# Performance work log

Hardware: AMD Instinct MI355X
Metric: run time of the kernel (lower is better)

Reference implementation:

```python
import jax, jax.numpy as jnp
import numpy as np

D_MODEL = 256
NHEAD = 8
NLAYERS = 4
DFF = 1024
PATCH = 8
INPUT = 32
C = 2
DATA_DIM = C * PATCH * PATCH  # 128
P = (INPUT // PATCH) ** 2     # 16
NEG = -1.0e6                  # _neg_large_for_dtype(float32)
EPS = 1e-5


def _ln(x, w, b):
    m = x.mean(-1, keepdims=True)
    v = ((x - m) ** 2).mean(-1, keepdims=True)
    return (x - m) / jnp.sqrt(v + EPS) * w + b


def _forward(img_baseline, acq_dts_float, nan_token, pad_embed, emb_w, emb_b, spatial_pos,
             t_w1, t_b1, t_w2, t_b2, t_w3, t_b3,
             in_proj_w, in_proj_b, out_proj_w, out_proj_b,
             lin1_w, lin1_b, lin2_w, lin2_b, norm1_w, norm1_b, norm2_w, norm2_b,
             mean_w1, mean_b1, mean_w2, mean_b2, lv_w1, lv_b1, lv_w2, lv_b2):
    B, T, Cc, Hh, Ww = img_baseline.shape
    p = PATCH
    gh, gw = Hh // p, Ww // p
    L = T * P
    frame_pad = jnp.all(img_baseline == -9999.0, axis=(2, 3, 4))  # (B,T)
    nan_pix = jnp.isnan(img_baseline)
    token = jnp.clip(nan_token, -10.0, 10.0).reshape(1, 1, Cc, 1, 1)
    x = jnp.clip(jnp.where(nan_pix, token, img_baseline), -10.0, 10.0)

    def patchify(a):  # b t c (h ph)(w pw) -> b t (h w) (c ph pw)
        return a.reshape(B, T, Cc, gh, p, gw, p).transpose(0, 1, 3, 5, 2, 4, 6).reshape(B, T, P, Cc * p * p)

    xp = patchify(x)
    seq_nan = patchify(nan_pix).all(-1).reshape(B, L)
    seq_pad = jnp.broadcast_to(frame_pad[:, :, None], (B, T, P)).reshape(B, L)

    # temporal MLP embedding
    t_in = jnp.where(jnp.isnan(acq_dts_float), 0.0, acq_dts_float)[..., None]  # (B,T,1)
    h = jax.nn.relu(t_in @ t_w1.T + t_b1)
    h = jax.nn.relu(h @ t_w2.T + t_b2)
    temb = h @ t_w3.T + t_b3  # (B,T,D)

    z = xp @ emb_w.T + emb_b + spatial_pos + temb[:, :, None, :]  # (B,T,P,D)
    z = z.reshape(B, L, D_MODEL)
    z = jnp.where(seq_pad[..., None], pad_embed, z)  # masked_scatter of pad_embed

    # additive attention mask: rows with NaN/pad patches are fully masked except diagonal
    masked_rows = seq_nan | seq_pad
    mask = jnp.broadcast_to(jnp.where(masked_rows[:, :, None], NEG, 0.0), (B, L, L))
    eye = jnp.eye(L, dtype=bool)
    mask = jnp.where(eye[None, :, :] & masked_rows[:, :, None], 0.0, mask)
    # key_padding_mask merged additively on key columns
    mask = mask + jnp.where(seq_pad[:, None, :], NEG, 0.0)
    mask = mask[:, None, :, :]  # (B,1,L,L), shared across heads

    dh = D_MODEL // NHEAD
    scale = 1.0 / np.sqrt(dh).astype(np.float32)
    for l in range(NLAYERS):
        qkv = z @ in_proj_w[l].T + in_proj_b[l]
        q, k, v = jnp.split(qkv, 3, axis=-1)
        q = q.reshape(B, L, NHEAD, dh).transpose(0, 2, 1, 3)
        k = k.reshape(B, L, NHEAD, dh).transpose(0, 2, 1, 3)
        v = v.reshape(B, L, NHEAD, dh).transpose(0, 2, 1, 3)
        scores = jnp.einsum('bhqd,bhkd->bhqk', q, k) * scale + mask
        attn = jax.nn.softmax(scores, axis=-1)
        o = jnp.einsum('bhqk,bhkd->bhqd', attn, v).transpose(0, 2, 1, 3).reshape(B, L, D_MODEL)
        o = o @ out_proj_w[l].T + out_proj_b[l]
        z = _ln(z + o, norm1_w[l], norm1_b[l])
        ff = jax.nn.relu(z @ lin1_w[l].T + lin1_b[l]) @ lin2_w[l].T + lin2_b[l]
        z = _ln(z + ff, norm2_w[l], norm2_b[l])

    mean = jnp.clip(jax.nn.relu(z @ mean_w1.T + mean_b1) @ mean_w2.T + mean_b2, -10.0, 10.0)
    logvar = jnp.clip(jax.nn.relu(z @ lv_w1.T + lv_b1) @ lv_w2.T + lv_b2, -10.0, 5.0)

    def unpatch(a):  # b t (h w)(c ph pw) -> b t c (h ph)(w pw)
        return a.reshape(B, T, gh, gw, Cc, p, p).transpose(0, 1, 4, 2, 5, 3, 6).reshape(B, T, Cc, Hh, Ww)

    mean = unpatch(mean.reshape(B, T, P, DATA_DIM))
    logvar = unpatch(logvar.reshape(B, T, P, DATA_DIM))
    return mean[:, -1], logvar[:, -1]


def setup_inputs() -> dict:
    key = jax.random.key(0)
    ks = iter(jax.random.split(key, 48))

    def rn(shape, scale=0.02):
        return jax.random.normal(next(ks), shape, dtype=jnp.float32) * scale

    B, T = 4, 64
    z = lambda s: jnp.zeros(s, jnp.float32)
    return {
        'img_baseline': jax.random.normal(next(ks), (B, T, C, INPUT, INPUT), dtype=jnp.float32),
        'acq_dts_float': jax.random.uniform(next(ks), (B, T), dtype=jnp.float32) * 3000.0,
        'nan_token': rn((C,)),
        'pad_embed': rn((1, 1, D_MODEL)),
        'emb_w': rn((D_MODEL, DATA_DIM)),
        'emb_b': z((D_MODEL,)),
        'spatial_pos': rn((1, 1, P, D_MODEL)),
        't_w1': rn((64, 1)), 't_b1': z((64,)),
        't_w2': rn((128, 64)), 't_b2': z((128,)),
        't_w3': rn((D_MODEL, 128)), 't_b3': z((D_MODEL,)),
        'in_proj_w': rn((NLAYERS, 3 * D_MODEL, D_MODEL)),
        'in_proj_b': z((NLAYERS, 3 * D_MODEL)),
        'out_proj_w': rn((NLAYERS, D_MODEL, D_MODEL)),
        'out_proj_b': z((NLAYERS, D_MODEL)),
        'lin1_w': rn((NLAYERS, DFF, D_MODEL)), 'lin1_b': z((NLAYERS, DFF)),
        'lin2_w': rn((NLAYERS, D_MODEL, DFF)), 'lin2_b': z((NLAYERS, D_MODEL)),
        'norm1_w': jnp.ones((NLAYERS, D_MODEL), jnp.float32), 'norm1_b': z((NLAYERS, D_MODEL)),
        'norm2_w': jnp.ones((NLAYERS, D_MODEL), jnp.float32), 'norm2_b': z((NLAYERS, D_MODEL)),
        'mean_w1': rn((DFF, D_MODEL)), 'mean_b1': z((DFF,)),
        'mean_w2': rn((DATA_DIM, DFF)), 'mean_b2': z((DATA_DIM,)),
        'lv_w1': rn((DFF, D_MODEL)), 'lv_b1': z((DFF,)),
        'lv_w2': rn((DATA_DIM, DFF)), 'lv_b2': z((DATA_DIM,)),
    }


def reference(img_baseline, acq_dts_float, nan_token, pad_embed, emb_w, emb_b, spatial_pos,
              t_w1, t_b1, t_w2, t_b2, t_w3, t_b3,
              in_proj_w, in_proj_b, out_proj_w, out_proj_b,
              lin1_w, lin1_b, lin2_w, lin2_b, norm1_w, norm1_b, norm2_w, norm2_b,
              mean_w1, mean_b1, mean_w2, mean_b2, lv_w1, lv_b1, lv_w2, lv_b2):
    return _forward(img_baseline, acq_dts_float, nan_token, pad_embed, emb_w, emb_b, spatial_pos,
                    t_w1, t_b1, t_w2, t_b2, t_w3, t_b3,
                    in_proj_w, in_proj_b, out_proj_w, out_proj_b,
                    lin1_w, lin1_b, lin2_w, lin2_b, norm1_w, norm1_b, norm2_w, norm2_b,
                    mean_w1, mean_b1, mean_w2, mean_b2, lv_w1, lv_b1, lv_w2, lv_b2)
```

## Files before the change

kernel.cpp:

```cpp
#include <hip/hip_runtime.h>
#include <hip/hip_bf16.h>

#define D_MODEL 256
#define NHEAD 8
#define DH 32
#define NLAYERS 4
#define DFF 1024
#define CC 2
#define DATA_DIM 128
#define PP 16
#define TT 64
#define BB 4
#define LL 1024
#define NEGV -1000000.0f

typedef __bf16 bf16_t;
typedef __bf16 bf16x8 __attribute__((ext_vector_type(8)));
typedef __bf16 bf16x4 __attribute__((ext_vector_type(4)));
typedef float v4f __attribute__((ext_vector_type(4)));

__device__ __forceinline__ bool my_isnan(float v) {
    unsigned u = __float_as_uint(v);
    return (u & 0x7fffffffu) > 0x7f800000u;
}

__device__ __forceinline__ void gld16(bf16_t* l, const bf16_t* g) {
    __builtin_amdgcn_global_load_lds(
        (const __attribute__((address_space(1))) void*)g,
        (__attribute__((address_space(3))) void*)l, 16, 0, 0);
}

__global__ __launch_bounds__(256) void f2b_prep_kernel(
    const float* __restrict__ in_proj_w, bf16_t* __restrict__ inb,
    const float* __restrict__ out_proj_w, bf16_t* __restrict__ outb,
    const float* __restrict__ lin1_w, bf16_t* __restrict__ l1b,
    const float* __restrict__ lin2_w, bf16_t* __restrict__ l2b,
    const float* __restrict__ emb_w, bf16_t* __restrict__ embwb,
    const float* __restrict__ mean_w1, const float* __restrict__ lv_w1, bf16_t* __restrict__ w1b,
    const float* __restrict__ mean_w2, const float* __restrict__ lv_w2, bf16_t* __restrict__ w2b,
    const float* __restrict__ img, const float* __restrict__ acq,
    const float* __restrict__ t_w1, const float* __restrict__ t_b1,
    const float* __restrict__ t_w2, const float* __restrict__ t_b2,
    const float* __restrict__ t_w3, const float* __restrict__ t_b3,
    float* __restrict__ temb, int* __restrict__ framepad) {
    const int n0 = NLAYERS * 768 * D_MODEL;
    const int n1 = NLAYERS * D_MODEL * D_MODEL;
    const int n2 = NLAYERS * DFF * D_MODEL;
    const int n3 = NLAYERS * D_MODEL * DFF;
    const int n4 = D_MODEL * DATA_DIM;
    const int n5 = DFF * D_MODEL;
    const int n6 = DFF * D_MODEL;
    const int n7 = DATA_DIM * DFF;
    const int n8 = DATA_DIM * DFF;
    int tid = threadIdx.x;
    int i = (blockIdx.x * 256 + tid) * 4;
    const float* s = nullptr; bf16_t* d = nullptr;
    if (i < n0) { s = in_proj_w; d = inb; }
    else if ((i -= n0) < n1) { s = out_proj_w; d = outb; }
    else if ((i -= n1) < n2) { s = lin1_w; d = l1b; }
    else if ((i -= n2) < n3) { s = lin2_w; d = l2b; }
    else if ((i -= n3) < n4) { s = emb_w; d = embwb; }
    else if ((i -= n4) < n5) { s = mean_w1; d = w1b; }
    else if ((i -= n5) < n6) { s = lv_w1; d = w1b + n5; }
    else if ((i -= n6) < n7) { s = mean_w2; d = w2b; }
    else if ((i -= n7) < n8) { s = lv_w2; d = w2b + n7; }
    if (s) {
        float4 v = *(const float4*)(s + i);
        bf16x4 o = {(bf16_t)v.x, (bf16_t)v.y, (bf16_t)v.z, (bf16_t)v.w};
        *(bf16x4*)(d + i) = o;
    }

    if (blockIdx.x >= BB * TT) return;
    int f = blockIdx.x;
    __shared__ float h1[64];
    __shared__ float h2[128];
    __shared__ int sAll;
    if (tid == 0) sAll = 1;
    __syncthreads();
    const float* fr = img + (size_t)f * (CC * 32 * 32);
    bool allpad = true;
    #pragma unroll
    for (int k = 0; k < 8; ++k) {
        float v = fr[tid + k * 256];
        allpad = allpad && (v == -9999.0f);
    }
    if (!allpad) sAll = 0;
    __syncthreads();
    if (tid == 0) framepad[f] = sAll;

    float t_in = acq[f];
    if (my_isnan(t_in)) t_in = 0.0f;
    if (tid < 64) h1[tid] = fmaxf(t_w1[tid] * t_in + t_b1[tid], 0.0f);
    __syncthreads();
    if (tid < 128) {
        float a = t_b2[tid];
        #pragma unroll 8
        for (int j = 0; j < 64; ++j) a += t_w2[tid * 64 + j] * h1[j];
        h2[tid] = fmaxf(a, 0.0f);
    }
    __syncthreads();
    {
        float a = t_b3[tid];
        #pragma unroll 8
        for (int j = 0; j < 128; ++j) a += t_w3[tid * 128 + j] * h2[j];
        temb[(size_t)f * D_MODEL + tid] = a;
    }
}

__global__ __launch_bounds__(256) void patchify_kernel(
    const float* __restrict__ img, const float* __restrict__ nan_token,
    const int* __restrict__ framepad,
    bf16_t* __restrict__ xpb, int* __restrict__ masked_rows,
    float* __restrict__ kmaskf) {
    int tid = threadIdx.x;
    int token = blockIdx.x * 2 + (tid >> 7);
    int dd = tid & 127;
    int l = token & 1023, b = token >> 10;
    int t = l >> 4, p = l & 15;
    int c = dd >> 6, pr = (dd >> 3) & 7, pc = dd & 7;
    int hh = (p >> 2) * 8 + pr, ww = (p & 3) * 8 + pc;
    float v = img[(((size_t)(b * TT + t) * CC + c) * 32 + hh) * 32 + ww];
    bool nanp = my_isnan(v);
    if (nanp) v = fminf(fmaxf(nan_token[c], -10.0f), 10.0f);
    v = fminf(fmaxf(v, -10.0f), 10.0f);
    xpb[(size_t)token * DATA_DIM + dd] = (bf16_t)v;

    __shared__ int wAll[4];
    unsigned long long bal = __ballot(nanp);
    if ((tid & 63) == 0) wAll[tid >> 6] = (bal == 0xFFFFFFFFFFFFFFFFull) ? 1 : 0;
    __syncthreads();
    if (tid < 2) {
        int tk = blockIdx.x * 2 + tid;
        int allnan = wAll[tid * 2] & wAll[tid * 2 + 1];
        int fp = framepad[tk >> 4];
        masked_rows[tk] = allnan | fp;
        kmaskf[tk] = fp ? NEGV : 0.0f;
    }
}

__global__ __launch_bounds__(256) void embed_gemm(
    const bf16_t* __restrict__ X, const bf16_t* __restrict__ W,
    const float* __restrict__ emb_b, const float* __restrict__ spatial,
    const float* __restrict__ temb, const float* __restrict__ pad_embed,
    const int* __restrict__ framepad,
    bf16_t* __restrict__ zb) {
    __shared__ __align__(16) bf16_t Xs[2][128 * 64];
    __shared__ __align__(16) bf16_t Ws[2][64 * 64];
    int tid = threadIdx.x;
    int wave = tid >> 6, lane = tid & 63;
    int quad = lane >> 4, l16 = lane & 15;
    int m0 = blockIdx.y * 128, n0 = blockIdx.x * 64;
    const int K = DATA_DIM, N = D_MODEL;

    v4f acc[2][4];
    #pragma unroll
    for (int i = 0; i < 2; ++i)
        #pragma unroll
        for (int j = 0; j < 4; ++j) acc[i][j] = (v4f){0.f, 0.f, 0.f, 0.f};

    int sr = tid >> 3, ss = tid & 7;
    int gc = (ss ^ (sr & 7)) * 8;

#define ESTAGE(bufi, k0)                                                          \
    do {                                                                          \
        _Pragma("unroll")                                                         \
        for (int p = 0; p < 4; ++p) {                                             \
            int r = sr + p * 32;                                                  \
            gld16(Xs[bufi] + r * 64 + ss * 8, X + (size_t)(m0 + r) * K + (k0) + gc); \
        }                                                                         \
        _Pragma("unroll")                                                         \
        for (int p = 0; p < 2; ++p) {                                             \
            int r = sr + p * 32;                                                  \
            gld16(Ws[bufi] + r * 64 + ss * 8, W + (size_t)(n0 + r) * K + (k0) + gc); \
        }                                                                         \
    } while (0)

    ESTAGE(0, 0);
    __syncthreads();
    const int T = K / 64;
    int swl = l16 & 7;
    for (int t = 0; t < T; ++t) {
        int buf = t & 1;
        if (t + 1 < T) ESTAGE(buf ^ 1, (t + 1) * 64);
        const bf16_t* Xc = Xs[buf];
        const bf16_t* Wc = Ws[buf];
        int ra = wave * 32 + l16;
        #pragma unroll
        for (int h = 0; h < 2; ++h) {
            int g8 = ((h * 4 + quad) ^ swl) * 8;
            bf16x8 af0 = *(const bf16x8*)(Xc + ra * 64 + g8);
            bf16x8 af1 = *(const bf16x8*)(Xc + (ra + 16) * 64 + g8);
            #pragma unroll
            for (int nt = 0; nt < 4; ++nt) {
                bf16x8 bfr = *(const bf16x8*)(Wc + (nt * 16 + l16) * 64 + g8);
                acc[0][nt] = __builtin_amdgcn_mfma_f32_16x16x32_bf16(af0, bfr, acc[0][nt], 0, 0, 0);
                acc[1][nt] = __builtin_amdgcn_mfma_f32_16x16x32_bf16(af1, bfr, acc[1][nt], 0, 0, 0);
            }
        }
        __syncthreads();
    }
#undef ESTAGE

    #pragma unroll
    for (int mt = 0; mt < 2; ++mt)
        #pragma unroll
        for (int nt = 0; nt < 4; ++nt) {
            int col = n0 + nt * 16 + l16;
            #pragma unroll
            for (int reg = 0; reg < 4; ++reg) {
                int row = m0 + wave * 32 + mt * 16 + quad * 4 + reg;
                int frame = row >> 4, p = row & 15;
                float v;
                if (framepad[frame]) {
                    v = pad_embed[col];
                } else {
                    v = acc[mt][nt][reg] + emb_b[col] + spatial[p * N + col]
                      + temb[(size_t)frame * N + col];
                }
                zb[(size_t)row * N + col] = (bf16_t)v;
            }
        }
}

template <int MODE, int RELU>
__global__ __launch_bounds__(256) void gemm_mfma(
    const bf16_t* __restrict__ X, const bf16_t* __restrict__ W,
    const float* __restrict__ bias, bf16_t* __restrict__ Y,
    bf16_t* __restrict__ Vt, int M, int N, int K) {
    __shared__ __align__(16) bf16_t Xs[2][128 * 64];
    __shared__ __align__(16) bf16_t Ws[2][64 * 64];
    int tid = threadIdx.x;
    int wave = tid >> 6, lane = tid & 63;
    int quad = lane >> 4, l16 = lane & 15;
    int m0 = blockIdx.y * 128, n0 = blockIdx.x * 64;

    v4f acc[2][4];
    #pragma unroll
    for (int i = 0; i < 2; ++i)
        #pragma unroll
        for (int j = 0; j < 4; ++j) acc[i][j] = (v4f){0.f, 0.f, 0.f, 0.f};

    int sr = tid >> 3, ss = tid & 7;
    int gc = (ss ^ (sr & 7)) * 8;

#define GSTAGE(bufi, k0)                                                          \
    do {                                                                          \
        _Pragma("unroll")                                                         \
        for (int p = 0; p < 4; ++p) {                                             \
            int r = sr + p * 32;                                                  \
            gld16(Xs[bufi] + r * 64 + ss * 8, X + (size_t)(m0 + r) * K + (k0) + gc); \
        }                                                                         \
        _Pragma("unroll")                                                         \
        for (int p = 0; p < 2; ++p) {                                             \
            int r = sr + p * 32;                                                  \
            gld16(Ws[bufi] + r * 64 + ss * 8, W + (size_t)(n0 + r) * K + (k0) + gc); \
        }                                                                         \
    } while (0)

    GSTAGE(0, 0);
    __syncthreads();
    const int T = K >> 6;
    int swl = l16 & 7;
    for (int t = 0; t < T; ++t) {
        int buf = t & 1;
        if (t + 1 < T) GSTAGE(buf ^ 1, (t + 1) * 64);
        const bf16_t* Xc = Xs[buf];
        const bf16_t* Wc = Ws[buf];
        int ra = wave * 32 + l16;
        #pragma unroll
        for (int h = 0; h < 2; ++h) {
            int g8 = ((h * 4 + quad) ^ swl) * 8;
            bf16x8 af0 = *(const bf16x8*)(Xc + ra * 64 + g8);
            bf16x8 af1 = *(const bf16x8*)(Xc + (ra + 16) * 64 + g8);
            #pragma unroll
            for (int nt = 0; nt < 4; ++nt) {
                bf16x8 bfr = *(const bf16x8*)(Wc + (nt * 16 + l16) * 64 + g8);
                acc[0][nt] = __builtin_amdgcn_mfma_f32_16x16x32_bf16(af0, bfr, acc[0][nt], 0, 0, 0);
                acc[1][nt] = __builtin_amdgcn_mfma_f32_16x16x32_bf16(af1, bfr, acc[1][nt], 0, 0, 0);
            }
        }
        __syncthreads();
    }
#undef GSTAGE

    if constexpr (MODE == 1) {
        #pragma unroll
        for (int mt = 0; mt < 2; ++mt)
            #pragma unroll
            for (int nt = 0; nt < 4; ++nt) {
                int col = n0 + nt * 16 + l16;
                float bv = bias[col];
                #pragma unroll
                for (int reg = 0; reg < 4; ++reg) {
                    int row = m0 + wave * 32 + mt * 16 + quad * 4 + reg;
                    float v = acc[mt][nt][reg] + bv;
                    if (RELU) v = fmaxf(v, 0.0f);
                    Y[(size_t)row * N + col] = (bf16_t)v;
                }
            }
    } else {
        if (n0 < 512) {
            #pragma unroll
            for (int mt = 0; mt < 2; ++mt)
                #pragma unroll
                for (int nt = 0; nt < 4; ++nt) {
                    int col = n0 + nt * 16 + l16;
                    float bv = bias[col];
                    #pragma unroll
                    for (int reg = 0; reg < 4; ++reg) {
                        int row = m0 + wave * 32 + mt * 16 + quad * 4 + reg;
                        float v = acc[mt][nt][reg] + bv;
                        Y[(size_t)row * 768 + col] = (bf16_t)v;
                    }
                }
        } else {
            bf16_t* VT = &Xs[0][0];
            #pragma unroll
            for (int mt = 0; mt < 2; ++mt)
                #pragma unroll
                for (int nt = 0; nt < 4; ++nt) {
                    int cl = nt * 16 + l16;
                    float bv = bias[n0 + cl];
                    #pragma unroll
                    for (int reg = 0; reg < 4; ++reg) {
                        int rl = wave * 32 + mt * 16 + quad * 4 + reg;
                        VT[cl * 136 + rl] = (bf16_t)(acc[mt][nt][reg] + bv);
                    }
                }
            __syncthreads();
            int b = m0 >> 10, l0m = m0 & 1023;
            int cl = tid >> 2;
            int rbase = (tid & 3) * 8;
            int cg2 = n0 + cl - 512;
            int h = cg2 >> 5, d = cg2 & 31;
            bf16_t* dst = Vt + (((size_t)(b * NHEAD + h)) * DH + d) * LL + l0m;
            #pragma unroll
            for (int u = 0; u < 4; ++u)
                *(uint4*)(dst + rbase + u * 32) = *(const uint4*)(VT + cl * 136 + rbase + u * 32);
        }
    }
}

__global__ __launch_bounds__(256) void gemm_row_ln(
    const bf16_t* __restrict__ X, const bf16_t* __restrict__ W,
    const float* __restrict__ bias, const bf16_t* __restrict__ Zres,
    bf16_t* __restrict__ Y, const float* __restrict__ lnw,
    const float* __restrict__ lnb, int K) {
    __shared__ __align__(16) bf16_t Xs[2][64 * 64];
    __shared__ __align__(16) bf16_t Ws[2][256 * 64];
    int tid = threadIdx.x;
    int wave = tid >> 6, lane = tid & 63;
    int quad = lane >> 4, l16 = lane & 15;
    int m0 = blockIdx.x * 64;

    v4f acc[16];
    #pragma unroll
    for (int j = 0; j < 16; ++j) acc[j] = (v4f){0.f, 0.f, 0.f, 0.f};

    int sr = tid >> 3, ss = tid & 7;
    int gc = (ss ^ (sr & 7)) * 8;

#define RSTAGE(bufi, k0)                                                          \
    do {                                                                          \
        _Pragma("unroll")                                                         \
        for (int p = 0; p < 2; ++p) {                                             \
            int r = sr + p * 32;                                                  \
            gld16(Xs[bufi] + r * 64 + ss * 8, X + (size_t)(m0 + r) * K + (k0) + gc); \
        }                                                                         \
        _Pragma("unroll")                                                         \
        for (int p = 0; p < 8; ++p) {                                             \
            int r = sr + p * 32;                                                  \
            gld16(Ws[bufi] + r * 64 + ss * 8, W + (size_t)r * K + (k0) + gc);     \
        }                                                                         \
    } while (0)

    RSTAGE(0, 0);
    __syncthreads();
    const int T = K >> 6;
    int swl = l16 & 7;
    for (int t = 0; t < T; ++t) {
        int buf = t & 1;
        if (t + 1 < T) RSTAGE(buf ^ 1, (t + 1) * 64);
        const bf16_t* Xc = Xs[buf];
        const bf16_t* Wc = Ws[buf];
        int ra = wave * 16 + l16;
        #pragma unroll
        for (int h = 0; h < 2; ++h) {
            int g8 = ((h * 4 + quad) ^ swl) * 8;
            bf16x8 af = *(const bf16x8*)(Xc + ra * 64 + g8);
            #pragma unroll
            for (int nt = 0; nt < 16; ++nt) {
                bf16x8 bfr = *(const bf16x8*)(Wc + (nt * 16 + l16) * 64 + g8);
                acc[nt] = __builtin_amdgcn_mfma_f32_16x16x32_bf16(af, bfr, acc[nt], 0, 0, 0);
            }
        }
        __syncthreads();
    }
#undef RSTAGE

    float wv[16], bvv[16];
    #pragma unroll
    for (int nt = 0; nt < 16; ++nt) {
        int col = nt * 16 + l16;
        float bv = bias[col];
        wv[nt] = lnw[col];
        bvv[nt] = lnb[col];
        #pragma unroll
        for (int reg = 0; reg < 4; ++reg) {
            int row = m0 + wave * 16 + quad * 4 + reg;
            acc[nt][reg] += bv + (float)Zres[(size_t)row * D_MODEL + col];
        }
    }
    #pragma unroll
    for (int reg = 0; reg < 4; ++reg) {
        float s = 0.0f;
        #pragma unroll
        for (int nt = 0; nt < 16; ++nt) s += acc[nt][reg];
        s += __shfl_xor(s, 1); s += __shfl_xor(s, 2);
        s += __shfl_xor(s, 4); s += __shfl_xor(s, 8);
        float mean = s * (1.0f / D_MODEL);
        float sq = 0.0f;
        #pragma unroll
        for (int nt = 0; nt < 16; ++nt) { float d = acc[nt][reg] - mean; sq += d * d; }
        sq += __shfl_xor(sq, 1); sq += __shfl_xor(sq, 2);
        sq += __shfl_xor(sq, 4); sq += __shfl_xor(sq, 8);
        float inv = 1.0f / sqrtf(sq * (1.0f / D_MODEL) + 1e-5f);
        int row = m0 + wave * 16 + quad * 4 + reg;
        #pragma unroll
        for (int nt = 0; nt < 16; ++nt) {
            int col = nt * 16 + l16;
            Y[(size_t)row * D_MODEL + col] =
                (bf16_t)((acc[nt][reg] - mean) * inv * wv[nt] + bvv[nt]);
        }
    }
}

__global__ __launch_bounds__(256) void attn_mfma(
    const bf16_t* __restrict__ qkvb, const bf16_t* __restrict__ Vt,
    const int* __restrict__ masked_rows, const float* __restrict__ kmaskf,
    bf16_t* __restrict__ Ob) {
    __shared__ __align__(16) bf16_t Ks[2][128 * 40];
    __shared__ __align__(16) bf16_t Vs[2][32 * 136];
    __shared__ __align__(16) float  Kms[2][128];
    __shared__ __align__(16) bf16_t Ps[4][16 * 136];

    int tid = threadIdx.x;
    int wave = tid >> 6, lane = tid & 63;
    int quad = lane >> 4, l16 = lane & 15;
    int bid = blockIdx.x;
    int h = bid & 7, b = (bid >> 3) & 3, qt = bid >> 5;
    int q0 = qt * 64 + wave * 16;
    const float scale = 0.17677669529663687f;

    bf16x8 qf = *(const bf16x8*)(qkvb + ((size_t)(b * LL) + q0 + l16) * 768 + h * DH + quad * 8);

    int mq = masked_rows[b * LL + q0 + l16];
    int qg = q0 + l16;

    float lrun = 0.0f;
    v4f oacc[2];
    oacc[0] = (v4f){0.f, 0.f, 0.f, 0.f};
    oacc[1] = (v4f){0.f, 0.f, 0.f, 0.f};

    int kr = tid >> 1, kh = (tid & 1) * 16;
    int vd = tid >> 3, vs0 = (tid & 7) * 8;
    const bf16_t* Kbase = qkvb + (size_t)(b * LL) * 768 + 256 + h * DH;
    const bf16_t* Vbase = Vt + (((size_t)(b * NHEAD + h)) * DH) * LL;
    const float* kmbase = kmaskf + b * LL;

    uint4 ka, kb, va, vb;
    float kmg;
    #define LOADC(c)                                                            \
        do {                                                                    \
            int _k0 = (c) * 128;                                                \
            ka = *(const uint4*)(Kbase + (size_t)(_k0 + kr) * 768 + kh);        \
            kb = *(const uint4*)(Kbase + (size_t)(_k0 + kr) * 768 + kh + 8);    \
            va = *(const uint4*)(Vbase + (size_t)vd * LL + _k0 + vs0);          \
            vb = *(const uint4*)(Vbase + (size_t)vd * LL + _k0 + 64 + vs0);     \
            kmg = (tid < 128) ? kmbase[_k0 + tid] : 0.0f;                       \
        } while (0)
    #define WRITEBUF(buf)                                                       \
        do {                                                                    \
            *(uint4*)(Ks[(buf)] + kr * 40 + kh) = ka;                           \
            *(uint4*)(Ks[(buf)] + kr * 40 + kh + 8) = kb;                       \
            *(uint4*)(Vs[(buf)] + vd * 136 + vs0) = va;                         \
            *(uint4*)(Vs[(buf)] + vd * 136 + 64 + vs0) = vb;                    \
            if (tid < 128) Kms[(buf)][tid] = kmg;                               \
        } while (0)

    LOADC(0);
    WRITEBUF(0);
    LOADC(1);

    bf16_t* Pw = Ps[wave];
    for (int c = 0; c < 8; ++c) {
        __syncthreads();
        int cur = c & 1;
        if (c + 1 < 8) WRITEBUF(cur ^ 1);
        if (c + 2 < 8) LOADC(c + 2);

        int k0 = c * 128;
        const bf16_t* Kc = Ks[cur];
        const bf16_t* Vc = Vs[cur];
        const float* kmc = Kms[cur];

        v4f sf[8];
        #pragma unroll
        for (int nt = 0; nt < 8; ++nt) {
            bf16x8 kf = *(const bf16x8*)(Kc + (nt * 16 + l16) * 40 + quad * 8);
            v4f zf = (v4f){0.f, 0.f, 0.f, 0.f};
            sf[nt] = __builtin_amdgcn_mfma_f32_16x16x32_bf16(kf, qf, zf, 0, 0, 0);
        }

        #pragma unroll
        for (int nt = 0; nt < 8; ++nt) {
            int kbase_nt = k0 + nt * 16 + quad * 4;
            float4 kmv = *(const float4*)(kmc + nt * 16 + quad * 4);
            float pv[4];
            #pragma unroll
            for (int reg = 0; reg < 4; ++reg) {
                float km = (reg == 0) ? kmv.x : (reg == 1) ? kmv.y : (reg == 2) ? kmv.z : kmv.w;
                float v = sf[nt][reg] * scale + km;
                if (mq && (qg != kbase_nt + reg)) v += NEGV;
                float p = __expf(v);
                lrun += p;
                pv[reg] = p;
            }
            bf16x4 pp = {(bf16_t)pv[0], (bf16_t)pv[1], (bf16_t)pv[2], (bf16_t)pv[3]};
            *(bf16x4*)(Pw + l16 * 136 + nt * 16 + quad * 4) = pp;
        }

        #pragma unroll
        for (int kt = 0; kt < 4; ++kt) {
            bf16x8 pf = *(const bf16x8*)(Pw + l16 * 136 + kt * 32 + quad * 8);
            #pragma unroll
            for (int nt2 = 0; nt2 < 2; ++nt2) {
                bf16x8 vf = *(const bf16x8*)(Vc + (nt2 * 16 + l16) * 136 + kt * 32 + quad * 8);
                oacc[nt2] = __builtin_amdgcn_mfma_f32_16x16x32_bf16(pf, vf, oacc[nt2], 0, 0, 0);
            }
        }
    }
    #undef LOADC
    #undef WRITEBUF

    lrun += __shfl_xor(lrun, 16);
    lrun += __shfl_xor(lrun, 32);
    float lq[4];
    #pragma unroll
    for (int reg = 0; reg < 4; ++reg) lq[reg] = __shfl(lrun, quad * 4 + reg);

    #pragma unroll
    for (int nt2 = 0; nt2 < 2; ++nt2)
        #pragma unroll
        for (int reg = 0; reg < 4; ++reg) {
            size_t row = (size_t)(b * LL) + q0 + quad * 4 + reg;
            Ob[row * 256 + h * DH + nt2 * 16 + l16] = (bf16_t)(oacc[nt2][reg] / lq[reg]);
        }
}

__global__ __launch_bounds__(256) void head_h_kernel(
    const bf16_t* __restrict__ zb, const bf16_t* __restrict__ W1b,
    const float* __restrict__ mean_b1, const float* __restrict__ lv_b1,
    bf16_t* __restrict__ hb) {
    __shared__ __align__(16) bf16_t Xs[2][64 * 64];
    __shared__ __align__(16) bf16_t Ws[2][64 * 64];
    int tid = threadIdx.x;
    int wave = tid >> 6, lane = tid & 63;
    int quad = lane >> 4, l16 = lane & 15;
    int head = blockIdx.y;
    int n0 = blockIdx.x * 64;
    const bf16_t* W1h = W1b + (size_t)head * DFF * D_MODEL;
    const float* B1f = head ? lv_b1 : mean_b1;
    bf16_t* hbh = hb + (size_t)head * 64 * DFF;

    v4f acc[4];
    #pragma unroll
    for (int j = 0; j < 4; ++j) acc[j] = (v4f){0.f, 0.f, 0.f, 0.f};

    int sr = tid >> 3, ss = tid & 7;
    int gc = (ss ^ (sr & 7)) * 8;

#define HSTAGE(bufi, k0)                                                          \
    do {                                                                          \
        _Pragma("unroll")                                                         \
        for (int p = 0; p < 2; ++p) {                                             \
            int r = sr + p * 32;                                                  \
            const bf16_t* xr = zb + (size_t)((r >> 4) * LL + (TT - 1) * PP + (r & 15)) * D_MODEL; \
            gld16(Xs[bufi] + r * 64 + ss * 8, xr + (k0) + gc);                    \
            gld16(Ws[bufi] + r * 64 + ss * 8, W1h + (size_t)(n0 + r) * D_MODEL + (k0) + gc); \
        }                                                                         \
    } while (0)

    HSTAGE(0, 0);
    __syncthreads();
    const int T = D_MODEL / 64;
    int swl = l16 & 7;
    for (int t = 0; t < T; ++t) {
        int buf = t & 1;
        if (t + 1 < T) HSTAGE(buf ^ 1, (t + 1) * 64);
        const bf16_t* Xc = Xs[buf];
        const bf16_t* Wc = Ws[buf];
        int ra = wave * 16 + l16;
        #pragma unroll
        for (int h = 0; h < 2; ++h) {
            int g8 = ((h * 4 + quad) ^ swl) * 8;
            bf16x8 af = *(const bf16x8*)(Xc + ra * 64 + g8);
            #pragma unroll
            for (int nt = 0; nt < 4; ++nt) {
                bf16x8 bfr = *(const bf16x8*)(Wc + (nt * 16 + l16) * 64 + g8);
                acc[nt] = __builtin_amdgcn_mfma_f32_16x16x32_bf16(af, bfr, acc[nt], 0, 0, 0);
            }
        }
        __syncthreads();
    }
#undef HSTAGE

    #pragma unroll
    for (int nt = 0; nt < 4; ++nt) {
        int col = n0 + nt * 16 + l16;
        float bv = B1f[col];
        #pragma unroll
        for (int reg = 0; reg < 4; ++reg) {
            int row = wave * 16 + quad * 4 + reg;
            hbh[(size_t)row * DFF + col] = (bf16_t)fmaxf(acc[nt][reg] + bv, 0.0f);
        }
    }
}

__global__ __launch_bounds__(256) void head_out_kernel(
    const bf16_t* __restrict__ hb, const bf16_t* __restrict__ W2b,
    const float* __restrict__ mean_b2, const float* __restrict__ lv_b2,
    float* __restrict__ out) {
    __shared__ __align__(16) bf16_t hrow[DFF];
    int tid = threadIdx.x;
    int bid = blockIdx.x;
    int head = bid >> 7, rr = (bid >> 1) & 63, half = bid & 1;
    int b = rr >> 4, p = rr & 15;

    if (tid < 128)
        *(uint4*)(hrow + tid * 8) =
            *(const uint4*)(hb + ((size_t)head * 64 + rr) * DFF + tid * 8);
    __syncthreads();

    int ol = tid >> 2, quarter = tid & 3;
    int o = half * 64 + ol;
    const bf16_t* wrow = W2b + ((size_t)head * DATA_DIM + o) * DFF + quarter * 256;
    const bf16_t* hseg = hrow + quarter * 256;
    float acc = 0.0f;
    #pragma unroll 8
    for (int j = 0; j < 32; ++j) {
        bf16x8 w = *(const bf16x8*)(wrow + j * 8);
        bf16x8 hv = *(const bf16x8*)(hseg + j * 8);
        #pragma unroll
        for (int e = 0; e < 8; ++e) acc += (float)w[e] * (float)hv[e];
    }
    acc += __shfl_xor(acc, 1);
    acc += __shfl_xor(acc, 2);
    if (quarter == 0) {
        const float* B2 = head ? lv_b2 : mean_b2;
        float hi = head ? 5.0f : 10.0f;
        float v = fminf(fmaxf(acc + B2[o], -10.0f), hi);
        int c = o >> 6;
        int pr = (o >> 3) & 7, pc = o & 7;
        int hh = (p >> 2) * 8 + pr, ww = (p & 3) * 8 + pc;
        out[(size_t)head * 8192 + ((size_t)(b * CC + c)) * 1024 + hh * 32 + ww] = v;
    }
}

extern "C" void kernel_launch(void* const* d_in, const int* in_sizes, int n_in,
                              void* d_out, int out_size, void* d_ws, size_t ws_size,
                              hipStream_t stream) {
    const float* img        = (const float*)d_in[0];
    const float* acq        = (const float*)d_in[1];
    const float* nan_token  = (const float*)d_in[2];
    const float* pad_embed  = (const float*)d_in[3];
    const float* emb_w      = (const float*)d_in[4];
    const float* emb_b      = (const float*)d_in[5];
    const float* spatial    = (const float*)d_in[6];
    const float* t_w1       = (const float*)d_in[7];
    const float* t_b1       = (const float*)d_in[8];
    const float* t_w2       = (const float*)d_in[9];
    const float* t_b2       = (const float*)d_in[10];
    const float* t_w3       = (const float*)d_in[11];
    const float* t_b3       = (const float*)d_in[12];
    const float* in_proj_w  = (const float*)d_in[13];
    const float* in_proj_b  = (const float*)d_in[14];
    const float* out_proj_w = (const float*)d_in[15];
    const float* out_proj_b = (const float*)d_in[16];
    const float* lin1_w     = (const float*)d_in[17];
    const float* lin1_b     = (const float*)d_in[18];
    const float* lin2_w     = (const float*)d_in[19];
    const float* lin2_b     = (const float*)d_in[20];
    const float* norm1_w    = (const float*)d_in[21];
    const float* norm1_b    = (const float*)d_in[22];
    const float* norm2_w    = (const float*)d_in[23];
    const float* norm2_b    = (const float*)d_in[24];
    const float* mean_w1    = (const float*)d_in[25];
    const float* mean_b1    = (const float*)d_in[26];
    const float* mean_w2    = (const float*)d_in[27];
    const float* mean_b2    = (const float*)d_in[28];
    const float* lv_w1      = (const float*)d_in[29];
    const float* lv_b1      = (const float*)d_in[30];
    const float* lv_w2      = (const float*)d_in[31];
    const float* lv_b2      = (const float*)d_in[32];

    const int M = BB * LL;

    char* wsb = (char*)d_ws;
    float* temb    = (float*)wsb;                    wsb += (size_t)BB * TT * D_MODEL * 4;
    float* kmaskf  = (float*)wsb;                    wsb += M * 4;
    int* framepad  = (int*)wsb;                      wsb += BB * TT * 4;
    int* masked    = (int*)wsb;                      wsb += M * 4;
    wsb = (char*)(((uintptr_t)wsb + 255) & ~(uintptr_t)255);
    bf16_t* zb     = (bf16_t*)wsb;                   wsb += (size_t)M * D_MODEL * 2;
    bf16_t* xpb    = (bf16_t*)wsb;                   wsb += (size_t)M * DATA_DIM * 2;
    bf16_t* qkvb   = (bf16_t*)wsb;                   wsb += (size_t)M * 768 * 2;
    bf16_t* VtG    = (bf16_t*)wsb;                   wsb += (size_t)M * D_MODEL * 2;
    bf16_t* attnb  = (bf16_t*)wsb;                   wsb += (size_t)M * D_MODEL * 2;
    bf16_t* ff1b   = (bf16_t*)wsb;                   wsb += (size_t)M * DFF * 2;
    bf16_t* inb    = (bf16_t*)wsb;                   wsb += (size_t)NLAYERS * 768 * D_MODEL * 2;
    bf16_t* outb   = (bf16_t*)wsb;                   wsb += (size_t)NLAYERS * D_MODEL * D_MODEL * 2;
    bf16_t* l1b    = (bf16_t*)wsb;                   wsb += (size_t)NLAYERS * DFF * D_MODEL * 2;
    bf16_t* l2b    = (bf16_t*)wsb;                   wsb += (size_t)NLAYERS * D_MODEL * DFF * 2;
    bf16_t* embwb  = (bf16_t*)wsb;                   wsb += (size_t)D_MODEL * DATA_DIM * 2;
    bf16_t* w1b    = (bf16_t*)wsb;                   wsb += (size_t)2 * DFF * D_MODEL * 2;
    bf16_t* w2b    = (bf16_t*)wsb;                   wsb += (size_t)2 * DATA_DIM * DFF * 2;
    bf16_t* hb     = (bf16_t*)wsb;                   wsb += (size_t)2 * 64 * DFF * 2;

    float* outF = (float*)d_out;

    {
        int tot = NLAYERS * 768 * D_MODEL + NLAYERS * D_MODEL * D_MODEL +
                  NLAYERS * DFF * D_MODEL + NLAYERS * D_MODEL * DFF +
                  D_MODEL * DATA_DIM + 2 * DFF * D_MODEL + 2 * DATA_DIM * DFF;
        f2b_prep_kernel<<<(tot / 4 + 255) / 256, 256, 0, stream>>>(
            in_proj_w, inb, out_proj_w, outb, lin1_w, l1b, lin2_w, l2b,
            emb_w, embwb, mean_w1, lv_w1, w1b, mean_w2, lv_w2, w2b,
            img, acq, t_w1, t_b1, t_w2, t_b2, t_w3, t_b3, temb, framepad);
    }

    patchify_kernel<<<M / 2, 256, 0, stream>>>(img, nan_token, framepad, xpb, masked, kmaskf);
    embed_gemm<<<dim3(D_MODEL / 64, M / 128), 256, 0, stream>>>(
        xpb, embwb, emb_b, spatial, temb, pad_embed, framepad, zb);

    for (int l = 0; l < NLAYERS; ++l) {
        gemm_mfma<2, 0><<<dim3(768 / 64, M / 128), 256, 0, stream>>>(
            zb, inb + (size_t)l * 768 * D_MODEL, in_proj_b + (size_t)l * 768,
            qkvb, VtG, M, 768, D_MODEL);
        attn_mfma<<<BB * NHEAD * (LL / 64), 256, 0, stream>>>(qkvb, VtG, masked, kmaskf, attnb);
        gemm_row_ln<<<M / 64, 256, 0, stream>>>(
            attnb, outb + (size_t)l * D_MODEL * D_MODEL, out_proj_b + (size_t)l * D_MODEL,
            zb, zb, norm1_w + l * D_MODEL, norm1_b + l * D_MODEL, D_MODEL);
        gemm_mfma<1, 1><<<dim3(DFF / 64, M / 128), 256, 0, stream>>>(
            zb, l1b + (size_t)l * DFF * D_MODEL, lin1_b + (size_t)l * DFF,
            ff1b, nullptr, M, DFF, D_MODEL);
        gemm_row_ln<<<M / 64, 256, 0, stream>>>(
            ff1b, l2b + (size_t)l * D_MODEL * DFF, lin2_b + (size_t)l * D_MODEL,
            zb, zb, norm2_w + l * D_MODEL, norm2_b + l * D_MODEL, DFF);
    }

    head_h_kernel<<<dim3(DFF / 64, 2), 256, 0, stream>>>(zb, w1b, mean_b1, lv_b1, hb);
    head_out_kernel<<<256, 256, 0, stream>>>(hb, w2b, mean_b2, lv_b2, outF);
}
```

Measured before the change: 440.4 us.

## Split row-LN GEMMs into tiled GEMM plus LayerNorm, add 3-stage LDS pipeline

The fused GEMM+LayerNorm kernel, which used one block per 64 full rows (only 64 blocks), is replaced by a 64x64-tiled residual GEMM writing to a temp buffer, followed by a separate wave-per-row LayerNorm kernel. The goal is more blocks and better CU occupancy for the out-proj and FFN2 projections. Both GEMMs also move from double to triple-buffered LDS staging with explicit vmcnt waits and one barrier per iteration. The cost is an extra kernel launch and a round trip of the activation through global memory per LN. Raw vmcnt counts must match the number of loads issued per stage.

```diff
diff --git a/kernel.cpp b/kernel.cpp
--- a/kernel.cpp
+++ b/kernel.cpp
@@ -227,8 +227,8 @@
     const bf16_t* __restrict__ X, const bf16_t* __restrict__ W,
     const float* __restrict__ bias, bf16_t* __restrict__ Y,
     bf16_t* __restrict__ Vt, int M, int N, int K) {
-    __shared__ __align__(16) bf16_t Xs[2][128 * 64];
-    __shared__ __align__(16) bf16_t Ws[2][64 * 64];
+    __shared__ __align__(16) bf16_t Xs[3][128 * 64];
+    __shared__ __align__(16) bf16_t Ws[3][64 * 64];
     int tid = threadIdx.x;
     int wave = tid >> 6, lane = tid & 63;
     int quad = lane >> 4, l16 = lane & 15;
@@ -257,13 +257,17 @@
         }                                                                         \
     } while (0)
 
+    const int T = K >> 6;
     GSTAGE(0, 0);
-    __syncthreads();
-    const int T = K >> 6;
+    if (T > 1) GSTAGE(1, 64);
     int swl = l16 & 7;
     for (int t = 0; t < T; ++t) {
-        int buf = t & 1;
-        if (t + 1 < T) GSTAGE(buf ^ 1, (t + 1) * 64);
+        int buf = t % 3;
+        if (t + 1 < T) asm volatile("s_waitcnt vmcnt(6)" ::: "memory");
+        else           asm volatile("s_waitcnt vmcnt(0)" ::: "memory");
+        __builtin_amdgcn_s_barrier();
+        __builtin_amdgcn_sched_barrier(0);
+        if (t + 2 < T) GSTAGE((t + 2) % 3, (t + 2) * 64);
         const bf16_t* Xc = Xs[buf];
         const bf16_t* Wc = Ws[buf];
         int ra = wave * 32 + l16;
@@ -279,9 +283,9 @@
                 acc[1][nt] = __builtin_amdgcn_mfma_f32_16x16x32_bf16(af1, bfr, acc[1][nt], 0, 0, 0);
             }
         }
-        __syncthreads();
     }
 #undef GSTAGE
+    __syncthreads();
 
     if constexpr (MODE == 1) {
         #pragma unroll
@@ -341,46 +345,45 @@
     }
 }
 
-__global__ __launch_bounds__(256) void gemm_row_ln(
+__global__ __launch_bounds__(256) void gemm_small(
     const bf16_t* __restrict__ X, const bf16_t* __restrict__ W,
     const float* __restrict__ bias, const bf16_t* __restrict__ Zres,
-    bf16_t* __restrict__ Y, const float* __restrict__ lnw,
-    const float* __restrict__ lnb, int K) {
-    __shared__ __align__(16) bf16_t Xs[2][64 * 64];
-    __shared__ __align__(16) bf16_t Ws[2][256 * 64];
+    bf16_t* __restrict__ Y, int M, int N, int K) {
+    __shared__ __align__(16) bf16_t Xs[3][64 * 64];
+    __shared__ __align__(16) bf16_t Ws[3][64 * 64];
     int tid = threadIdx.x;
     int wave = tid >> 6, lane = tid & 63;
     int quad = lane >> 4, l16 = lane & 15;
-    int m0 = blockIdx.x * 64;
-
-    v4f acc[16];
-    #pragma unroll
-    for (int j = 0; j < 16; ++j) acc[j] = (v4f){0.f, 0.f, 0.f, 0.f};
+    int m0 = blockIdx.y * 64, n0 = blockIdx.x * 64;
+
+    v4f acc[4];
+    #pragma unroll
+    for (int j = 0; j < 4; ++j) acc[j] = (v4f){0.f, 0.f, 0.f, 0.f};
 
     int sr = tid >> 3, ss = tid & 7;
     int gc = (ss ^ (sr & 7)) * 8;
 
-#define RSTAGE(bufi, k0)                                                          \
+#define SSTAGE(bufi, k0)                                                          \
     do {                                                                          \
         _Pragma("unroll")                                                         \
         for (int p = 0; p < 2; ++p) {                                             \
             int r = sr + p * 32;                                                  \
             gld16(Xs[bufi] + r * 64 + ss * 8, X + (size_t)(m0 + r) * K + (k0) + gc); \
-        }                                                                         \
-        _Pragma("unroll")                                                         \
-        for (int p = 0; p < 8; ++p) {                                             \
-            int r = sr + p * 32;                                                  \
-            gld16(Ws[bufi] + r * 64 + ss * 8, W + (size_t)r * K + (k0) + gc);     \
+            gld16(Ws[bufi] + r * 64 + ss * 8, W + (size_t)(n0 + r) * K + (k0) + gc); \
         }                                                                         \
     } while (0)
 
-    RSTAGE(0, 0);
-    __syncthreads();
     const int T = K >> 6;
+    SSTAGE(0, 0);
+    if (T > 1) SSTAGE(1, 64);
     int swl = l16 & 7;
     for (int t = 0; t < T; ++t) {
-        int buf = t & 1;
-        if (t + 1 < T) RSTAGE(buf ^ 1, (t + 1) * 64);
+        int buf = t % 3;
+        if (t + 1 < T) asm volatile("s_waitcnt vmcnt(4)" ::: "memory");
+        else           asm volatile("s_waitcnt vmcnt(0)" ::: "memory");
+        __builtin_amdgcn_s_barrier();
+        __builtin_amdgcn_sched_barrier(0);
+        if (t + 2 < T) SSTAGE((t + 2) % 3, (t + 2) * 64);
         const bf16_t* Xc = Xs[buf];
         const bf16_t* Wc = Ws[buf];
         int ra = wave * 16 + l16;
@@ -389,48 +392,23 @@
             int g8 = ((h * 4 + quad) ^ swl) * 8;
             bf16x8 af = *(const bf16x8*)(Xc + ra * 64 + g8);
             #pragma unroll
-            for (int nt = 0; nt < 16; ++nt) {
+            for (int nt = 0; nt < 4; ++nt) {
                 bf16x8 bfr = *(const bf16x8*)(Wc + (nt * 16 + l16) * 64 + g8);
                 acc[nt] = __builtin_amdgcn_mfma_f32_16x16x32_bf16(af, bfr, acc[nt], 0, 0, 0);
             }
         }
-        __syncthreads();
-    }
-#undef RSTAGE
-
-    float wv[16], bvv[16];
-    #pragma unroll
-    for (int nt = 0; nt < 16; ++nt) {
-        int col = nt * 16 + l16;
+    }
+#undef SSTAGE
+
+    #pragma unroll
+    for (int nt = 0; nt < 4; ++nt) {
+        int col = n0 + nt * 16 + l16;
         float bv = bias[col];
-        wv[nt] = lnw[col];
-        bvv[nt] = lnb[col];
         #pragma unroll
         for (int reg = 0; reg < 4; ++reg) {
             int row = m0 + wave * 16 + quad * 4 + reg;
-            acc[nt][reg] += bv + (float)Zres[(size_t)row * D_MODEL + col];
-        }
-    }
-    #pragma unroll
-    for (int reg = 0; reg < 4; ++reg) {
-        float s = 0.0f;
-        #pragma unroll
-        for (int nt = 0; nt < 16; ++nt) s += acc[nt][reg];
-        s += __shfl_xor(s, 1); s += __shfl_xor(s, 2);
-        s += __shfl_xor(s, 4); s += __shfl_xor(s, 8);
-        float mean = s * (1.0f / D_MODEL);
-        float sq = 0.0f;
-        #pragma unroll
-        for (int nt = 0; nt < 16; ++nt) { float d = acc[nt][reg] - mean; sq += d * d; }
-        sq += __shfl_xor(sq, 1); sq += __shfl_xor(sq, 2);
-        sq += __shfl_xor(sq, 4); sq += __shfl_xor(sq, 8);
-        float inv = 1.0f / sqrtf(sq * (1.0f / D_MODEL) + 1e-5f);
-        int row = m0 + wave * 16 + quad * 4 + reg;
-        #pragma unroll
-        for (int nt = 0; nt < 16; ++nt) {
-            int col = nt * 16 + l16;
-            Y[(size_t)row * D_MODEL + col] =
-                (bf16_t)((acc[nt][reg] - mean) * inv * wv[nt] + bvv[nt]);
+            float r = acc[nt][reg] + bv + (float)Zres[(size_t)row * N + col];
+            Y[(size_t)row * N + col] = (bf16_t)r;
         }
     }
 }
@@ -558,12 +536,37 @@
         }
 }
 
+__global__ __launch_bounds__(256) void ln_kernel(
+    const bf16_t* __restrict__ tmps, const float* __restrict__ w,
+    const float* __restrict__ b, bf16_t* __restrict__ zb) {
+    int wave = threadIdx.x >> 6, lane = threadIdx.x & 63;
+    int row = blockIdx.x * 4 + wave;
+    bf16x4 xb = *(const bf16x4*)(tmps + (size_t)row * D_MODEL + lane * 4);
+    float x0 = (float)xb[0], x1 = (float)xb[1], x2 = (float)xb[2], x3 = (float)xb[3];
+    float s = x0 + x1 + x2 + x3;
+    #pragma unroll
+    for (int off = 32; off > 0; off >>= 1) s += __shfl_xor(s, off);
+    float mean = s * (1.0f / D_MODEL);
+    float dx0 = x0 - mean, dx1 = x1 - mean, dx2 = x2 - mean, dx3 = x3 - mean;
+    float sq = dx0 * dx0 + dx1 * dx1 + dx2 * dx2 + dx3 * dx3;
+    #pragma unroll
+    for (int off = 32; off > 0; off >>= 1) sq += __shfl_xor(sq, off);
+    float inv = 1.0f / sqrtf(sq * (1.0f / D_MODEL) + 1e-5f);
+    float4 wv = ((const float4*)w)[lane];
+    float4 bv = ((const float4*)b)[lane];
+    bf16x4 rb = {(bf16_t)(dx0 * inv * wv.x + bv.x),
+                 (bf16_t)(dx1 * inv * wv.y + bv.y),
+                 (bf16_t)(dx2 * inv * wv.z + bv.z),
+                 (bf16_t)(dx3 * inv * wv.w + bv.w)};
+    *(bf16x4*)(zb + (size_t)row * D_MODEL + lane * 4) = rb;
+}
+
 __global__ __launch_bounds__(256) void head_h_kernel(
     const bf16_t* __restrict__ zb, const bf16_t* __restrict__ W1b,
     const float* __restrict__ mean_b1, const float* __restrict__ lv_b1,
     bf16_t* __restrict__ hb) {
-    __shared__ __align__(16) bf16_t Xs[2][64 * 64];
-    __shared__ __align__(16) bf16_t Ws[2][64 * 64];
+    __shared__ __align__(16) bf16_t Xs[2][64 * 32 * 2];
+    __shared__ __align__(16) bf16_t Ws[2][64 * 32 * 2];
     int tid = threadIdx.x;
     int wave = tid >> 6, lane = tid & 63;
     int quad = lane >> 4, l16 = lane & 15;
@@ -713,6 +716,7 @@
     int* masked    = (int*)wsb;                      wsb += M * 4;
     wsb = (char*)(((uintptr_t)wsb + 255) & ~(uintptr_t)255);
     bf16_t* zb     = (bf16_t*)wsb;                   wsb += (size_t)M * D_MODEL * 2;
+    bf16_t* tmps   = (bf16_t*)wsb;                   wsb += (size_t)M * D_MODEL * 2;
     bf16_t* xpb    = (bf16_t*)wsb;                   wsb += (size_t)M * DATA_DIM * 2;
     bf16_t* qkvb   = (bf16_t*)wsb;                   wsb += (size_t)M * 768 * 2;
     bf16_t* VtG    = (bf16_t*)wsb;                   wsb += (size_t)M * D_MODEL * 2;
@@ -748,15 +752,19 @@
             zb, inb + (size_t)l * 768 * D_MODEL, in_proj_b + (size_t)l * 768,
             qkvb, VtG, M, 768, D_MODEL);
         attn_mfma<<<BB * NHEAD * (LL / 64), 256, 0, stream>>>(qkvb, VtG, masked, kmaskf, attnb);
-        gemm_row_ln<<<M / 64, 256, 0, stream>>>(
+        gemm_small<<<dim3(D_MODEL / 64, M / 64), 256, 0, stream>>>(
             attnb, outb + (size_t)l * D_MODEL * D_MODEL, out_proj_b + (size_t)l * D_MODEL,
-            zb, zb, norm1_w + l * D_MODEL, norm1_b + l * D_MODEL, D_MODEL);
+            zb, tmps, M, D_MODEL, D_MODEL);
+        ln_kernel<<<M / 4, 256, 0, stream>>>(tmps, norm1_w + l * D_MODEL,
+                                             norm1_b + l * D_MODEL, zb);
         gemm_mfma<1, 1><<<dim3(DFF / 64, M / 128), 256, 0, stream>>>(
             zb, l1b + (size_t)l * DFF * D_MODEL, lin1_b + (size_t)l * DFF,
             ff1b, nullptr, M, DFF, D_MODEL);
-        gemm_row_ln<<<M / 64, 256, 0, stream>>>(
+        gemm_small<<<dim3(D_MODEL / 64, M / 64), 256, 0, stream>>>(
             ff1b, l2b + (size_t)l * D_MODEL * DFF, lin2_b + (size_t)l * D_MODEL,
-            zb, zb, norm2_w + l * D_MODEL, norm2_b + l * D_MODEL, DFF);
+            zb, tmps, M, D_MODEL, DFF);
+        ln_kernel<<<M / 4, 256, 0, stream>>>(tmps, norm2_w + l * D_MODEL,
+                                             norm2_b + l * D_MODEL, zb);
     }
 
     head_h_kernel<<<dim3(DFF / 64, 2), 256, 0, stream>>>(zb, w1b, mean_b1, lv_b1, hb);
```

Measured after the change: 388.8 us (median of 2 runs). -11.7%, faster.

## Triple-buffer GEMM staging and split row-LN GEMM into 16-row blocks

Applied to the files above, without the earlier changes.

Both gemm_mfma and gemm_row_ln move from a two-stage to a three-stage shared-memory pipeline. They wait on explicit vmcnt counts and use a single barrier per k-step instead of two __syncthreads. gemm_row_ln now handles 16 rows per block, with the four waves splitting the 256 output columns, which gives four times as many blocks to fill the GPU at M=4096. The LayerNorm reductions therefore go through shared memory across waves and need extra barriers. Each block also reloads the full weight tile for fewer rows, which raises total weight traffic.

```diff
diff --git a/kernel.cpp b/kernel.cpp
--- a/kernel.cpp
+++ b/kernel.cpp
@@ -227,8 +227,8 @@
     const bf16_t* __restrict__ X, const bf16_t* __restrict__ W,
     const float* __restrict__ bias, bf16_t* __restrict__ Y,
     bf16_t* __restrict__ Vt, int M, int N, int K) {
-    __shared__ __align__(16) bf16_t Xs[2][128 * 64];
-    __shared__ __align__(16) bf16_t Ws[2][64 * 64];
+    __shared__ __align__(16) bf16_t Xs[3][128 * 64];
+    __shared__ __align__(16) bf16_t Ws[3][64 * 64];
     int tid = threadIdx.x;
     int wave = tid >> 6, lane = tid & 63;
     int quad = lane >> 4, l16 = lane & 15;
@@ -257,13 +257,17 @@
         }                                                                         \
     } while (0)
 
+    const int T = K >> 6;
     GSTAGE(0, 0);
-    __syncthreads();
-    const int T = K >> 6;
+    if (T > 1) GSTAGE(1, 64);
     int swl = l16 & 7;
     for (int t = 0; t < T; ++t) {
-        int buf = t & 1;
-        if (t + 1 < T) GSTAGE(buf ^ 1, (t + 1) * 64);
+        int buf = t % 3;
+        if (t + 1 < T) asm volatile("s_waitcnt vmcnt(6)" ::: "memory");
+        else           asm volatile("s_waitcnt vmcnt(0)" ::: "memory");
+        __builtin_amdgcn_s_barrier();
+        __builtin_amdgcn_sched_barrier(0);
+        if (t + 2 < T) GSTAGE((t + 2) % 3, (t + 2) * 64);
         const bf16_t* Xc = Xs[buf];
         const bf16_t* Wc = Ws[buf];
         int ra = wave * 32 + l16;
@@ -279,9 +283,9 @@
                 acc[1][nt] = __builtin_amdgcn_mfma_f32_16x16x32_bf16(af1, bfr, acc[1][nt], 0, 0, 0);
             }
         }
-        __syncthreads();
     }
 #undef GSTAGE
+    __syncthreads();
 
     if constexpr (MODE == 1) {
         #pragma unroll
@@ -346,27 +350,28 @@
     const float* __restrict__ bias, const bf16_t* __restrict__ Zres,
     bf16_t* __restrict__ Y, const float* __restrict__ lnw,
     const float* __restrict__ lnb, int K) {
-    __shared__ __align__(16) bf16_t Xs[2][64 * 64];
-    __shared__ __align__(16) bf16_t Ws[2][256 * 64];
+    __shared__ __align__(16) bf16_t Xs[3][16 * 64];
+    __shared__ __align__(16) bf16_t Ws[3][256 * 64];
     int tid = threadIdx.x;
     int wave = tid >> 6, lane = tid & 63;
     int quad = lane >> 4, l16 = lane & 15;
-    int m0 = blockIdx.x * 64;
-
-    v4f acc[16];
-    #pragma unroll
-    for (int j = 0; j < 16; ++j) acc[j] = (v4f){0.f, 0.f, 0.f, 0.f};
+    int mrow0 = blockIdx.x * 16;
+
+    v4f acc[4];
+    #pragma unroll
+    for (int j = 0; j < 4; ++j) acc[j] = (v4f){0.f, 0.f, 0.f, 0.f};
 
     int sr = tid >> 3, ss = tid & 7;
     int gc = (ss ^ (sr & 7)) * 8;
+    int xl = lane & 31;
+    int xrow = wave * 4 + (xl >> 3);
+    int xgc = ((xl & 7) ^ (xrow & 7)) * 8;
 
 #define RSTAGE(bufi, k0)                                                          \
     do {                                                                          \
-        _Pragma("unroll")                                                         \
-        for (int p = 0; p < 2; ++p) {                                             \
-            int r = sr + p * 32;                                                  \
-            gld16(Xs[bufi] + r * 64 + ss * 8, X + (size_t)(m0 + r) * K + (k0) + gc); \
-        }                                                                         \
+        if (lane < 32)                                                            \
+            gld16(Xs[bufi] + wave * 256 + xl * 8,                                 \
+                  X + (size_t)(mrow0 + xrow) * K + (k0) + xgc);                   \
         _Pragma("unroll")                                                         \
         for (int p = 0; p < 8; ++p) {                                             \
             int r = sr + p * 32;                                                  \
@@ -374,63 +379,101 @@
         }                                                                         \
     } while (0)
 
+    const int T = K >> 6;
     RSTAGE(0, 0);
-    __syncthreads();
-    const int T = K >> 6;
+    RSTAGE(1, 64);
     int swl = l16 & 7;
     for (int t = 0; t < T; ++t) {
-        int buf = t & 1;
-        if (t + 1 < T) RSTAGE(buf ^ 1, (t + 1) * 64);
+        int buf = t % 3;
+        if (t + 1 < T) asm volatile("s_waitcnt vmcnt(9)" ::: "memory");
+        else           asm volatile("s_waitcnt vmcnt(0)" ::: "memory");
+        __builtin_amdgcn_s_barrier();
+        __builtin_amdgcn_sched_barrier(0);
+        if (t + 2 < T) RSTAGE((t + 2) % 3, (t + 2) * 64);
         const bf16_t* Xc = Xs[buf];
         const bf16_t* Wc = Ws[buf];
-        int ra = wave * 16 + l16;
         #pragma unroll
         for (int h = 0; h < 2; ++h) {
             int g8 = ((h * 4 + quad) ^ swl) * 8;
-            bf16x8 af = *(const bf16x8*)(Xc + ra * 64 + g8);
-            #pragma unroll
-            for (int nt = 0; nt < 16; ++nt) {
+            bf16x8 af = *(const bf16x8*)(Xc + l16 * 64 + g8);
+            #pragma unroll
+            for (int ntl = 0; ntl < 4; ++ntl) {
+                int nt = wave * 4 + ntl;
                 bf16x8 bfr = *(const bf16x8*)(Wc + (nt * 16 + l16) * 64 + g8);
-                acc[nt] = __builtin_amdgcn_mfma_f32_16x16x32_bf16(af, bfr, acc[nt], 0, 0, 0);
+                acc[ntl] = __builtin_amdgcn_mfma_f32_16x16x32_bf16(af, bfr, acc[ntl], 0, 0, 0);
             }
         }
-        __syncthreads();
     }
 #undef RSTAGE
-
-    float wv[16], bvv[16];
-    #pragma unroll
-    for (int nt = 0; nt < 16; ++nt) {
-        int col = nt * 16 + l16;
+    __syncthreads();
+
+    float* psum = (float*)&Xs[0][0];
+    float xv[4][4];
+    float lw[4], lb[4];
+    #pragma unroll
+    for (int ntl = 0; ntl < 4; ++ntl) {
+        int col = wave * 64 + ntl * 16 + l16;
         float bv = bias[col];
-        wv[nt] = lnw[col];
-        bvv[nt] = lnb[col];
+        lw[ntl] = lnw[col];
+        lb[ntl] = lnb[col];
         #pragma unroll
         for (int reg = 0; reg < 4; ++reg) {
-            int row = m0 + wave * 16 + quad * 4 + reg;
-            acc[nt][reg] += bv + (float)Zres[(size_t)row * D_MODEL + col];
-        }
-    }
+            int grow = mrow0 + quad * 4 + reg;
+            xv[ntl][reg] = acc[ntl][reg] + bv + (float)Zres[(size_t)grow * D_MODEL + col];
+        }
+    }
+    float s[4];
     #pragma unroll
     for (int reg = 0; reg < 4; ++reg) {
-        float s = 0.0f;
-        #pragma unroll
-        for (int nt = 0; nt < 16; ++nt) s += acc[nt][reg];
-        s += __shfl_xor(s, 1); s += __shfl_xor(s, 2);
-        s += __shfl_xor(s, 4); s += __shfl_xor(s, 8);
-        float mean = s * (1.0f / D_MODEL);
-        float sq = 0.0f;
-        #pragma unroll
-        for (int nt = 0; nt < 16; ++nt) { float d = acc[nt][reg] - mean; sq += d * d; }
-        sq += __shfl_xor(sq, 1); sq += __shfl_xor(sq, 2);
-        sq += __shfl_xor(sq, 4); sq += __shfl_xor(sq, 8);
-        float inv = 1.0f / sqrtf(sq * (1.0f / D_MODEL) + 1e-5f);
-        int row = m0 + wave * 16 + quad * 4 + reg;
-        #pragma unroll
-        for (int nt = 0; nt < 16; ++nt) {
-            int col = nt * 16 + l16;
-            Y[(size_t)row * D_MODEL + col] =
-                (bf16_t)((acc[nt][reg] - mean) * inv * wv[nt] + bvv[nt]);
+        s[reg] = xv[0][reg] + xv[1][reg] + xv[2][reg] + xv[3][reg];
+        s[reg] += __shfl_xor(s[reg], 1);
+        s[reg] += __shfl_xor(s[reg], 2);
+        s[reg] += __shfl_xor(s[reg], 4);
+        s[reg] += __shfl_xor(s[reg], 8);
+    }
+    if (l16 == 0) {
+        #pragma unroll
+        for (int reg = 0; reg < 4; ++reg)
+            psum[wave * 16 + quad * 4 + reg] = s[reg];
+    }
+    __syncthreads();
+    float mean[4];
+    #pragma unroll
+    for (int reg = 0; reg < 4; ++reg) {
+        int row = quad * 4 + reg;
+        mean[reg] = (psum[row] + psum[16 + row] + psum[32 + row] + psum[48 + row])
+                  * (1.0f / D_MODEL);
+    }
+    __syncthreads();
+    float q[4];
+    #pragma unroll
+    for (int reg = 0; reg < 4; ++reg) {
+        float d0 = xv[0][reg] - mean[reg], d1 = xv[1][reg] - mean[reg];
+        float d2 = xv[2][reg] - mean[reg], d3 = xv[3][reg] - mean[reg];
+        q[reg] = d0 * d0 + d1 * d1 + d2 * d2 + d3 * d3;
+        q[reg] += __shfl_xor(q[reg], 1);
+        q[reg] += __shfl_xor(q[reg], 2);
+        q[reg] += __shfl_xor(q[reg], 4);
+        q[reg] += __shfl_xor(q[reg], 8);
+    }
+    if (l16 == 0) {
+        #pragma unroll
+        for (int reg = 0; reg < 4; ++reg)
+            psum[wave * 16 + quad * 4 + reg] = q[reg];
+    }
+    __syncthreads();
+    #pragma unroll
+    for (int reg = 0; reg < 4; ++reg) {
+        int row = quad * 4 + reg;
+        float var = (psum[row] + psum[16 + row] + psum[32 + row] + psum[48 + row])
+                  * (1.0f / D_MODEL);
+        float inv = 1.0f / sqrtf(var + 1e-5f);
+        int grow = mrow0 + row;
+        #pragma unroll
+        for (int ntl = 0; ntl < 4; ++ntl) {
+            int col = wave * 64 + ntl * 16 + l16;
+            Y[(size_t)grow * D_MODEL + col] =
+                (bf16_t)((xv[ntl][reg] - mean[reg]) * inv * lw[ntl] + lb[ntl]);
         }
     }
 }
@@ -562,8 +605,8 @@
     const bf16_t* __restrict__ zb, const bf16_t* __restrict__ W1b,
     const float* __restrict__ mean_b1, const float* __restrict__ lv_b1,
     bf16_t* __restrict__ hb) {
-    __shared__ __align__(16) bf16_t Xs[2][64 * 64];
-    __shared__ __align__(16) bf16_t Ws[2][64 * 64];
+    __shared__ __align__(16) bf16_t Xs[2][64 * 32 * 2];
+    __shared__ __align__(16) bf16_t Ws[2][64 * 32 * 2];
     int tid = threadIdx.x;
     int wave = tid >> 6, lane = tid & 63;
     int quad = lane >> 4, l16 = lane & 15;
@@ -748,13 +791,13 @@
             zb, inb + (size_t)l * 768 * D_MODEL, in_proj_b + (size_t)l * 768,
             qkvb, VtG, M, 768, D_MODEL);
         attn_mfma<<<BB * NHEAD * (LL / 64), 256, 0, stream>>>(qkvb, VtG, masked, kmaskf, attnb);
-        gemm_row_ln<<<M / 64, 256, 0, stream>>>(
+        gemm_row_ln<<<M / 16, 256, 0, stream>>>(
             attnb, outb + (size_t)l * D_MODEL * D_MODEL, out_proj_b + (size_t)l * D_MODEL,
             zb, zb, norm1_w + l * D_MODEL, norm1_b + l * D_MODEL, D_MODEL);
         gemm_mfma<1, 1><<<dim3(DFF / 64, M / 128), 256, 0, stream>>>(
             zb, l1b + (size_t)l * DFF * D_MODEL, lin1_b + (size_t)l * DFF,
             ff1b, nullptr, M, DFF, D_MODEL);
-        gemm_row_ln<<<M / 64, 256, 0, stream>>>(
+        gemm_row_ln<<<M / 16, 256, 0, stream>>>(
             ff1b, l2b + (size_t)l * D_MODEL * DFF, lin2_b + (size_t)l * D_MODEL,
             zb, zb, norm2_w + l * D_MODEL, norm2_b + l * D_MODEL, DFF);
     }
```

After: 389.8 us. -11.5%, faster.
